# Performance work log

Hardware: AMD Instinct MI355X
Metric: run time of the kernel (lower is better)

The kernel has to match this reference:

```python
import jax, jax.numpy as jnp
import numpy as np

NEG_SLOPE = 0.2
NEG_INF = -1e9


def _gat_branch(x, src, dst, edge_type, t, W, a_src, a_dst, b):
    """Single-head PyG GATConv restricted (by masking) to edges with edge_type == t,
    with self-loops added (PyG default add_self_loops=True)."""
    N = x.shape[0]
    h = x @ W                                   # [N, out_dim]
    s = h @ a_src                               # [N] source attention term
    d = h @ a_dst                               # [N] destination attention term
    # real edges (masked by type)
    e_edge = jax.nn.leaky_relu(s[src] + d[dst], NEG_SLOPE)
    e_edge = jnp.where(edge_type == t, e_edge, NEG_INF)
    # self-loop edges i -> i
    e_self = jax.nn.leaky_relu(s + d, NEG_SLOPE)
    dst_all = jnp.concatenate([dst, jnp.arange(N)])          # [E+N]
    e_all = jnp.concatenate([e_edge, e_self])                 # [E+N]
    # softmax over incoming edges per destination node (segment softmax)
    m = jax.ops.segment_max(e_all, dst_all, num_segments=N)
    p = jnp.exp(e_all - m[dst_all])
    denom = jax.ops.segment_sum(p, dst_all, num_segments=N)
    alpha = p / denom[dst_all]                                 # [E+N]
    msg = jnp.concatenate([h[src], h], axis=0) * alpha[:, None]
    return jax.ops.segment_sum(msg, dst_all, num_segments=N) + b


def setup_inputs() -> dict:
    key = jax.random.key(0)
    ks = jax.random.split(key, 12)
    N, E, in_dim, out_dim = 100000, 1000000, 64, 64
    glorot = (6.0 / (in_dim + out_dim)) ** 0.5
    att = (6.0 / (1 + out_dim)) ** 0.5
    return {
        "x": jax.random.normal(ks[0], (N, in_dim), dtype=jnp.float32),
        "edge_index": jax.random.randint(ks[1], (2, E), 0, N),
        "edge_type": jax.random.randint(ks[2], (E,), 0, 2),
        "W_login": jax.random.uniform(ks[3], (in_dim, out_dim), jnp.float32, -glorot, glorot),
        "a_src_login": jax.random.uniform(ks[4], (out_dim,), jnp.float32, -att, att),
        "a_dst_login": jax.random.uniform(ks[5], (out_dim,), jnp.float32, -att, att),
        "b_login": jnp.zeros((out_dim,), jnp.float32),
        "W_exec": jax.random.uniform(ks[6], (in_dim, out_dim), jnp.float32, -glorot, glorot),
        "a_src_exec": jax.random.uniform(ks[7], (out_dim,), jnp.float32, -att, att),
        "a_dst_exec": jax.random.uniform(ks[8], (out_dim,), jnp.float32, -att, att),
        "b_exec": jnp.zeros((out_dim,), jnp.float32),
    }


def reference(x, edge_index, edge_type, W_login, a_src_login, a_dst_login, b_login,
              W_exec, a_src_exec, a_dst_exec, b_exec):
    src, dst = edge_index[0], edge_index[1]
    out = _gat_branch(x, src, dst, edge_type, 0, W_login, a_src_login, a_dst_login, b_login)
    out = out + _gat_branch(x, src, dst, edge_type, 1, W_exec, a_src_exec, a_dst_exec, b_exec)
    return out
```

## Files before the change

kernel.cpp:

```cpp
#include <hip/hip_runtime.h>

#define D 64
#define CAP 896
#define BINB 256

typedef unsigned short u16;
typedef __attribute__((ext_vector_type(8))) __bf16 bf16x8;
typedef __attribute__((ext_vector_type(4))) float f32x4;

__device__ __forceinline__ float lrelu(float x) { return x > 0.f ? x : 0.2f * x; }
__device__ __forceinline__ u16 f2bf(float f) {
    unsigned u = __float_as_uint(f);
    return (u16)((u + 0x7fffu + ((u >> 16) & 1u)) >> 16);
}
__device__ __forceinline__ float bf2f(u16 v) { return __uint_as_float((unsigned)v << 16); }
__device__ __forceinline__ unsigned pack2(float lo, float hi) {
    return (unsigned)f2bf(lo) | ((unsigned)f2bf(hi) << 16);
}
__device__ __forceinline__ float blo(unsigned u) { return __uint_as_float(u << 16); }
__device__ __forceinline__ float bhi(unsigned u) { return __uint_as_float(u & 0xffff0000u); }

__global__ __launch_bounds__(256) void k_gemm3(
    const float* __restrict__ x,
    const float* __restrict__ W0, const float* __restrict__ as0, const float* __restrict__ ad0,
    const float* __restrict__ W1, const float* __restrict__ as1, const float* __restrict__ ad1,
    u16* __restrict__ hb, float* __restrict__ s_tab, float* __restrict__ d_tab,
    int N, int ntiles)
{
    __shared__ u16 Wb[2][64][64];
    __shared__ u16 Xb[64][72];
    __shared__ float wsd[4][64];

    const int tid = threadIdx.x;

    for (int i = tid; i < 4096; i += 256) {
        const int k = i >> 6, n = i & 63;
        Wb[0][n][k] = f2bf(W0[i]);
        Wb[1][n][k] = f2bf(W1[i]);
    }
    {
        const int k = tid & 63;
        const int v = tid >> 6;
        const float* Ws = (v < 2) ? W0 : W1;
        const float* av = (v == 0) ? as0 : (v == 1) ? ad0 : (v == 2) ? as1 : ad1;
        float q = 0.f;
        for (int n = 0; n < 64; ++n) q = fmaf(Ws[(k << 6) + n], av[n], q);
        wsd[v][k] = q;
    }
    __syncthreads();

    const int lane = tid & 63;
    const int nl = lane & 15, quad = lane >> 4;
    const int wv = tid >> 6;

    bf16x8 bfrag[2][4][2];
#pragma unroll
    for (int br = 0; br < 2; ++br)
#pragma unroll
        for (int t = 0; t < 4; ++t)
#pragma unroll
            for (int h = 0; h < 2; ++h)
                bfrag[br][t][h] = *(const bf16x8*)&Wb[br][t * 16 + nl][h * 32 + quad * 8];

    const int rstage = tid >> 2;
    const int kc = (tid & 3) << 4;

    for (int tile = blockIdx.x; tile < ntiles; tile += gridDim.x) {
        const long n0 = (long)tile << 6;
        __syncthreads();
        {
            long row = n0 + rstage; if (row >= N) row = N - 1;
            const float4* xp = (const float4*)(x + row * D + kc);
            const float4 v0 = xp[0], v1 = xp[1], v2 = xp[2], v3 = xp[3];

            unsigned q[8];
            q[0] = pack2(v0.x, v0.y); q[1] = pack2(v0.z, v0.w);
            q[2] = pack2(v1.x, v1.y); q[3] = pack2(v1.z, v1.w);
            q[4] = pack2(v2.x, v2.y); q[5] = pack2(v2.z, v2.w);
            q[6] = pack2(v3.x, v3.y); q[7] = pack2(v3.z, v3.w);
            *(uint4*)&Xb[rstage][kc]     = make_uint4(q[0], q[1], q[2], q[3]);
            *(uint4*)&Xb[rstage][kc + 8] = make_uint4(q[4], q[5], q[6], q[7]);

            float ps[4];
#pragma unroll
            for (int v = 0; v < 4; ++v) {
                const float4* wp = (const float4*)&wsd[v][kc];
                const float4 wa = wp[0], wb = wp[1], wc = wp[2], wd = wp[3];
                float s = 0.f;
                s = fmaf(v0.x, wa.x, s); s = fmaf(v0.y, wa.y, s);
                s = fmaf(v0.z, wa.z, s); s = fmaf(v0.w, wa.w, s);
                s = fmaf(v1.x, wb.x, s); s = fmaf(v1.y, wb.y, s);
                s = fmaf(v1.z, wb.z, s); s = fmaf(v1.w, wb.w, s);
                s = fmaf(v2.x, wc.x, s); s = fmaf(v2.y, wc.y, s);
                s = fmaf(v2.z, wc.z, s); s = fmaf(v2.w, wc.w, s);
                s = fmaf(v3.x, wd.x, s); s = fmaf(v3.y, wd.y, s);
                s = fmaf(v3.z, wd.z, s); s = fmaf(v3.w, wd.w, s);
                ps[v] = s;
            }
#pragma unroll
            for (int v = 0; v < 4; ++v) {
                ps[v] += __shfl_xor(ps[v], 1, 64);
                ps[v] += __shfl_xor(ps[v], 2, 64);
            }
            const long rw = n0 + rstage;
            if ((tid & 3) == 0 && rw < N) {
                s_tab[(rw << 1)]     = ps[0]; d_tab[(rw << 1)]     = ps[1];
                s_tab[(rw << 1) | 1] = ps[2]; d_tab[(rw << 1) | 1] = ps[3];
            }
        }
        __syncthreads();

        const int rbase = wv << 4;
        const bf16x8 a0 = *(const bf16x8*)&Xb[rbase + nl][quad * 8];
        const bf16x8 a1 = *(const bf16x8*)&Xb[rbase + nl][32 + quad * 8];

        f32x4 acc[2][4];
#pragma unroll
        for (int br = 0; br < 2; ++br)
#pragma unroll
            for (int t = 0; t < 4; ++t) {
                f32x4 c = {0.f, 0.f, 0.f, 0.f};
                c = __builtin_amdgcn_mfma_f32_16x16x32_bf16(a0, bfrag[br][t][0], c, 0, 0, 0);
                c = __builtin_amdgcn_mfma_f32_16x16x32_bf16(a1, bfrag[br][t][1], c, 0, 0, 0);
                acc[br][t] = c;
            }

#pragma unroll
        for (int reg = 0; reg < 4; ++reg) {
            const long row = n0 + rbase + (quad << 2) + reg;
            if (row < N) {
#pragma unroll
                for (int br = 0; br < 2; ++br) {
                    uint2 v;
                    v.x = pack2(acc[br][0][reg], acc[br][1][reg]);
                    v.y = pack2(acc[br][2][reg], acc[br][3][reg]);
                    *(uint2*)(hb + (((row << 1) | br) << 6) + (nl << 2)) = v;
                }
            }
        }
    }
}

__global__ __launch_bounds__(256) void k_bin1(
    const int* __restrict__ src, const int* __restrict__ dst,
    const int* __restrict__ et, int* __restrict__ bktcnt,
    unsigned* __restrict__ bkt, int E, int nbk, int Eseg)
{
    extern __shared__ int cnt_l[];
    const int tid = threadIdx.x;
    for (int i = tid; i < nbk; i += 256) cnt_l[i] = 0;
    __syncthreads();

    const long e0 = (long)blockIdx.x * Eseg;
    const long e1 = min(e0 + (long)Eseg, (long)E);

    long i = e0 + tid;
    for (; i + 256 * 7 < e1; i += 256 * 8) {
        int d[8];
#pragma unroll
        for (int k = 0; k < 8; ++k) d[k] = dst[i + 256 * k];
#pragma unroll
        for (int k = 0; k < 8; ++k) atomicAdd(&cnt_l[d[k] >> 6], 1);
    }
    for (; i < e1; i += 256) atomicAdd(&cnt_l[dst[i] >> 6], 1);
    __syncthreads();

    for (int j = tid; j < nbk; j += 256) {
        const int c = cnt_l[j];
        cnt_l[j] = c ? atomicAdd(bktcnt + j, c) : 0;
    }
    __syncthreads();

    i = e0 + tid;
    for (; i + 256 * 7 < e1; i += 256 * 8) {
        int d[8];
#pragma unroll
        for (int k = 0; k < 8; ++k) d[k] = dst[i + 256 * k];
#pragma unroll
        for (int k = 0; k < 8; ++k) {
            const int bb = d[k] >> 6;
            const long ii = i + 256 * k;
            const int slot = atomicAdd(&cnt_l[bb], 1);
            if (slot < CAP)
                bkt[(long)bb * CAP + slot] =
                    ((unsigned)(d[k] & 63) << 18) | ((unsigned)src[ii] << 1) | (unsigned)et[ii];
        }
    }
    for (; i < e1; i += 256) {
        const int d = dst[i];
        const int bb = d >> 6;
        const int slot = atomicAdd(&cnt_l[bb], 1);
        if (slot < CAP)
            bkt[(long)bb * CAP + slot] =
                ((unsigned)(d & 63) << 18) | ((unsigned)src[i] << 1) | (unsigned)et[i];
    }
}

__global__ __launch_bounds__(512) void k_proc(
    const int* __restrict__ bktcnt, const unsigned* __restrict__ bkt,
    const float* __restrict__ s_tab, const float* __restrict__ d_tab,
    const u16* __restrict__ hb,
    const float* __restrict__ b0, const float* __restrict__ b1,
    float* __restrict__ out, int N)
{
    __shared__ unsigned tok[CAP];
    __shared__ int degl[64];
    __shared__ int curl[64];
    __shared__ float bsum[64];

    const int tid = threadIdx.x;
    const int b = blockIdx.x;
    const int lo = b << 6;
    const int cnt_nodes = min(64, N - lo);
    const int nb = min(bktcnt[b], CAP);

    if (tid < 64) { degl[tid] = 0; bsum[tid] = b0[tid] + b1[tid]; }
    __syncthreads();

    unsigned pr[2];
    int ns = 0;
    for (int i = tid; i < nb; i += 512) {
        const unsigned p = bkt[(long)b * CAP + i];
        pr[ns++] = p;
        atomicAdd(&degl[(p >> 18) & 63], 1);
    }
    __syncthreads();
    if (tid < 64) {
        int v = degl[tid];
        const int orig = v;
#pragma unroll
        for (int o = 1; o < 64; o <<= 1) {
            const int u = __shfl_up(v, o, 64);
            if (tid >= o) v += u;
        }
        curl[tid] = v - orig;
    }
    __syncthreads();
    for (int k = 0, i = tid; k < ns; i += 512, ++k) {
        const unsigned p = pr[k];
        const int s = atomicAdd(&curl[(p >> 18) & 63], 1);
        tok[s] = p & 0x3FFFFu;
    }
    __syncthreads();

    const int lane = tid & 63;
    const int wave = tid >> 6;
    const int q = lane >> 4;
    const int cl = lane & 15;

    for (int ni = wave; ni < cnt_nodes; ni += 8) {
        const int n = lo + ni;
        const int deg = degl[ni];
        const int off = curl[ni] - deg;
        const float d0n = d_tab[(n << 1)];
        const float d1n = d_tab[(n << 1) | 1];

        if (deg <= 62) {
            const int cnt = deg + 2;
            unsigned cmb = 0; unsigned t = 0; float e = 0.f;
            if (lane < deg) {
                cmb = tok[off + lane];
                t = cmb & 1u;
                e = lrelu(s_tab[cmb] + (t ? d1n : d0n));
            } else if (lane == deg)   { cmb = (unsigned)(n << 1);      t = 0; e = lrelu(s_tab[cmb] + d0n); }
            else if (lane == deg + 1) { cmb = (unsigned)(n << 1) | 1u; t = 1; e = lrelu(s_tab[cmb] + d1n); }

            const bool act = lane < cnt;
            const float p = act ? __expf(e) : 0.f;
            float p0 = t ? 0.f : p;
            float p1 = t ? p : 0.f;
#pragma unroll
            for (int o = 32; o; o >>= 1) {
                p0 += __shfl_xor(p0, o, 64);
                p1 += __shfl_xor(p1, o, 64);
            }
            const float a_r = act ? p / (t ? p1 : p0) : 0.f;

            float4 acc = {0.f, 0.f, 0.f, 0.f};
            const int nq = (cnt + 3) >> 2;
            int pp = 0;
            for (; pp + 1 < nq; pp += 2) {
                const int iA = (pp << 2) + q;
                const int iB = iA + 4;
                const int iBc = iB < cnt ? iB : cnt - 1;
                float aA    = __shfl(a_r, iA, 64);
                unsigned cA = __shfl(cmb, iA, 64);
                float aB    = __shfl(a_r, iBc, 64);
                unsigned cB = __shfl(cmb, iBc, 64);
                if (iB >= cnt) aB = 0.f;
                const uint2 uA = *(const uint2*)(hb + ((long)cA << 6) + (cl << 2));
                const uint2 uB = *(const uint2*)(hb + ((long)cB << 6) + (cl << 2));
                acc.x = fmaf(aA, blo(uA.x), acc.x);
                acc.y = fmaf(aA, bhi(uA.x), acc.y);
                acc.z = fmaf(aA, blo(uA.y), acc.z);
                acc.w = fmaf(aA, bhi(uA.y), acc.w);
                acc.x = fmaf(aB, blo(uB.x), acc.x);
                acc.y = fmaf(aB, bhi(uB.x), acc.y);
                acc.z = fmaf(aB, blo(uB.y), acc.z);
                acc.w = fmaf(aB, bhi(uB.y), acc.w);
            }
            if (pp < nq) {
                const int iA = (pp << 2) + q;
                const int iAc = iA < cnt ? iA : cnt - 1;
                float aA    = __shfl(a_r, iAc, 64);
                unsigned cA = __shfl(cmb, iAc, 64);
                if (iA >= cnt) aA = 0.f;
                const uint2 uA = *(const uint2*)(hb + ((long)cA << 6) + (cl << 2));
                acc.x = fmaf(aA, blo(uA.x), acc.x);
                acc.y = fmaf(aA, bhi(uA.x), acc.y);
                acc.z = fmaf(aA, blo(uA.y), acc.z);
                acc.w = fmaf(aA, bhi(uA.y), acc.w);
            }
            acc.x += __shfl_xor(acc.x, 16, 64);
            acc.y += __shfl_xor(acc.y, 16, 64);
            acc.z += __shfl_xor(acc.z, 16, 64);
            acc.w += __shfl_xor(acc.w, 16, 64);
            acc.x += __shfl_xor(acc.x, 32, 64);
            acc.y += __shfl_xor(acc.y, 32, 64);
            acc.z += __shfl_xor(acc.z, 32, 64);
            acc.w += __shfl_xor(acc.w, 32, 64);
            if (lane < 16) {
                float* op = out + ((long)n << 6);
                op[cl]      = acc.x + bsum[cl];
                op[16 + cl] = acc.y + bsum[16 + cl];
                op[32 + cl] = acc.z + bsum[32 + cl];
                op[48 + cl] = acc.w + bsum[48 + cl];
            }
        } else {
            const int oc = ((lane & 3) << 4) + (lane >> 2);
            const float es0 = lrelu(s_tab[(n << 1)] + d0n);
            const float es1 = lrelu(s_tab[(n << 1) | 1] + d1n);
            float p0 = 0.f, p1 = 0.f;
            for (int j = lane; j < deg; j += 64) {
                const unsigned c = tok[off + j];
                const float e = lrelu(s_tab[c] + ((c & 1u) ? d1n : d0n));
                if (c & 1u) p1 += __expf(e); else p0 += __expf(e);
            }
#pragma unroll
            for (int o = 32; o; o >>= 1) {
                p0 += __shfl_xor(p0, o, 64);
                p1 += __shfl_xor(p1, o, 64);
            }
            const float den0 = p0 + __expf(es0);
            const float den1 = p1 + __expf(es1);

            float acc = (__expf(es0) / den0) * bf2f(hb[((long)n << 7) + lane])
                      + (__expf(es1) / den1) * bf2f(hb[((long)n << 7) + 64 + lane]);
            for (int base = 0; base < deg; base += 64) {
                const int j = base + lane;
                unsigned ck = 0; float a = 0.f;
                if (j < deg) {
                    ck = tok[off + j];
                    const float e = lrelu(s_tab[ck] + ((ck & 1u) ? d1n : d0n));
                    a = __expf(e) / ((ck & 1u) ? den1 : den0);
                }
                const int lim = min(64, deg - base);
                for (int jj = 0; jj < lim; ++jj) {
                    const float aj = __shfl(a, jj, 64);
                    const unsigned cj = __shfl(ck, jj, 64);
                    acc = fmaf(aj, bf2f(hb[((long)cj << 6) + lane]), acc);
                }
            }
            out[((long)n << 6) + oc] = acc + bsum[oc];
        }
    }
}

extern "C" void kernel_launch(void* const* d_in, const int* in_sizes, int n_in,
                              void* d_out, int out_size, void* d_ws, size_t ws_size,
                              hipStream_t stream) {
    const float* x   = (const float*)d_in[0];
    const int*   ei  = (const int*)d_in[1];
    const int*   et  = (const int*)d_in[2];
    const float* W0  = (const float*)d_in[3];
    const float* as0 = (const float*)d_in[4];
    const float* ad0 = (const float*)d_in[5];
    const float* b0  = (const float*)d_in[6];
    const float* W1  = (const float*)d_in[7];
    const float* as1 = (const float*)d_in[8];
    const float* ad1 = (const float*)d_in[9];
    const float* b1  = (const float*)d_in[10];
    float* out = (float*)d_out;

    const int N = in_sizes[0] / D;
    const int E = in_sizes[1] / 2;
    const int* src = ei;
    const int* dst = ei + E;

    const int nbk = (N + 63) >> 6;

    char* w = (char*)d_ws;
    u16* hb = (u16*)w;            w += (size_t)2 * N * D * sizeof(u16);
    float* s_tab = (float*)w;     w += (size_t)2 * N * sizeof(float);
    float* d_tab = (float*)w;     w += (size_t)2 * N * sizeof(float);
    int* bktcnt = (int*)w;        w += (size_t)nbk * sizeof(int);
    unsigned* bkt = (unsigned*)w; w += (size_t)nbk * CAP * sizeof(unsigned);

    const int ntiles = (N + 63) / 64;
    const int Eseg = (E + BINB - 1) / BINB;

    hipMemsetAsync(bktcnt, 0, (size_t)nbk * sizeof(int), stream);
    k_gemm3<<<768, 256, 0, stream>>>(x, W0, as0, ad0, W1, as1, ad1,
                                     hb, s_tab, d_tab, N, ntiles);
    k_bin1<<<BINB, 256, (size_t)nbk * sizeof(int), stream>>>(
        src, dst, et, bktcnt, bkt, E, nbk, Eseg);
    k_proc<<<nbk, 512, 0, stream>>>(bktcnt, bkt, s_tab, d_tab, hb, b0, b1, out, N);
}
```

Baseline: 195.0 us.

## Fuse GEMM and edge binning into one front kernel; widen gather loads

Merges the projection GEMM kernel and the edge-binning kernel into a single 768-block kernel. Each block runs its GEMM tiles, then reuses the weight shared memory as local bucket counters and bins its edge segment, which removes one launch and spreads binning over more blocks. The aggregation kernel now has each lane gather 8 bf16 features with a 16-byte load instead of 4 with an 8-byte load, so 8 edges are processed per step. It also adds a nontemporal load for bucket tokens. The trade-offs are a longer shuffle reduction, more registers, and the reused shared memory (16 KB) capping nbk at 4096, which leaves little headroom above the ~1563 buckets needed here.

```diff
diff --git a/kernel.cpp b/kernel.cpp
--- a/kernel.cpp
+++ b/kernel.cpp
@@ -2,7 +2,7 @@
 
 #define D 64
 #define CAP 896
-#define BINB 256
+#define FRONT_BLKS 768
 
 typedef unsigned short u16;
 typedef __attribute__((ext_vector_type(8))) __bf16 bf16x8;
@@ -20,12 +20,14 @@
 __device__ __forceinline__ float blo(unsigned u) { return __uint_as_float(u << 16); }
 __device__ __forceinline__ float bhi(unsigned u) { return __uint_as_float(u & 0xffff0000u); }
 
-__global__ __launch_bounds__(256) void k_gemm3(
+__global__ __launch_bounds__(256) void k_front(
     const float* __restrict__ x,
     const float* __restrict__ W0, const float* __restrict__ as0, const float* __restrict__ ad0,
     const float* __restrict__ W1, const float* __restrict__ as1, const float* __restrict__ ad1,
     u16* __restrict__ hb, float* __restrict__ s_tab, float* __restrict__ d_tab,
-    int N, int ntiles)
+    const int* __restrict__ src, const int* __restrict__ dst, const int* __restrict__ et,
+    int* __restrict__ bktcnt, unsigned* __restrict__ bkt,
+    int E, int nbk, int Eseg, int N, int ntiles)
 {
     __shared__ u16 Wb[2][64][64];
     __shared__ u16 Xb[64][72];
@@ -65,7 +67,7 @@
     const int rstage = tid >> 2;
     const int kc = (tid & 3) << 4;
 
-    for (int tile = blockIdx.x; tile < ntiles; tile += gridDim.x) {
+    for (int tile = blockIdx.x; tile < ntiles; tile += FRONT_BLKS) {
         const long n0 = (long)tile << 6;
         __syncthreads();
         {
@@ -139,15 +141,9 @@
             }
         }
     }
-}
-
-__global__ __launch_bounds__(256) void k_bin1(
-    const int* __restrict__ src, const int* __restrict__ dst,
-    const int* __restrict__ et, int* __restrict__ bktcnt,
-    unsigned* __restrict__ bkt, int E, int nbk, int Eseg)
-{
-    extern __shared__ int cnt_l[];
-    const int tid = threadIdx.x;
+
+    __syncthreads();
+    int* cnt_l = (int*)&Wb[0][0][0];
     for (int i = tid; i < nbk; i += 256) cnt_l[i] = 0;
     __syncthreads();
 
@@ -220,7 +216,7 @@
     unsigned pr[2];
     int ns = 0;
     for (int i = tid; i < nb; i += 512) {
-        const unsigned p = bkt[(long)b * CAP + i];
+        const unsigned p = __builtin_nontemporal_load(&bkt[(long)b * CAP + i]);
         pr[ns++] = p;
         atomicAdd(&degl[(p >> 18) & 63], 1);
     }
@@ -245,8 +241,8 @@
 
     const int lane = tid & 63;
     const int wave = tid >> 6;
-    const int q = lane >> 4;
-    const int cl = lane & 15;
+    const int q8 = lane >> 3;
+    const int c8 = lane & 7;
 
     for (int ni = wave; ni < cnt_nodes; ni += 8) {
         const int n = lo + ni;
@@ -276,55 +272,54 @@
             }
             const float a_r = act ? p / (t ? p1 : p0) : 0.f;
 
-            float4 acc = {0.f, 0.f, 0.f, 0.f};
-            const int nq = (cnt + 3) >> 2;
+            float acc[8] = {0.f, 0.f, 0.f, 0.f, 0.f, 0.f, 0.f, 0.f};
+            const int no = (cnt + 7) >> 3;
             int pp = 0;
-            for (; pp + 1 < nq; pp += 2) {
-                const int iA = (pp << 2) + q;
-                const int iB = iA + 4;
+            for (; pp + 1 < no; pp += 2) {
+                const int iA = (pp << 3) + q8;
+                const int iB = iA + 8;
                 const int iBc = iB < cnt ? iB : cnt - 1;
                 float aA    = __shfl(a_r, iA, 64);
                 unsigned cA = __shfl(cmb, iA, 64);
                 float aB    = __shfl(a_r, iBc, 64);
                 unsigned cB = __shfl(cmb, iBc, 64);
                 if (iB >= cnt) aB = 0.f;
-                const uint2 uA = *(const uint2*)(hb + ((long)cA << 6) + (cl << 2));
-                const uint2 uB = *(const uint2*)(hb + ((long)cB << 6) + (cl << 2));
-                acc.x = fmaf(aA, blo(uA.x), acc.x);
-                acc.y = fmaf(aA, bhi(uA.x), acc.y);
-                acc.z = fmaf(aA, blo(uA.y), acc.z);
-                acc.w = fmaf(aA, bhi(uA.y), acc.w);
-                acc.x = fmaf(aB, blo(uB.x), acc.x);
-                acc.y = fmaf(aB, bhi(uB.x), acc.y);
-                acc.z = fmaf(aB, blo(uB.y), acc.z);
-                acc.w = fmaf(aB, bhi(uB.y), acc.w);
-            }
-            if (pp < nq) {
-                const int iA = (pp << 2) + q;
+                const uint4 uA = *(const uint4*)(hb + ((long)cA << 6) + (c8 << 3));
+                const uint4 uB = *(const uint4*)(hb + ((long)cB << 6) + (c8 << 3));
+                acc[0] = fmaf(aA, blo(uA.x), acc[0]); acc[1] = fmaf(aA, bhi(uA.x), acc[1]);
+                acc[2] = fmaf(aA, blo(uA.y), acc[2]); acc[3] = fmaf(aA, bhi(uA.y), acc[3]);
+                acc[4] = fmaf(aA, blo(uA.z), acc[4]); acc[5] = fmaf(aA, bhi(uA.z), acc[5]);
+                acc[6] = fmaf(aA, blo(uA.w), acc[6]); acc[7] = fmaf(aA, bhi(uA.w), acc[7]);
+                acc[0] = fmaf(aB, blo(uB.x), acc[0]); acc[1] = fmaf(aB, bhi(uB.x), acc[1]);
+                acc[2] = fmaf(aB, blo(uB.y), acc[2]); acc[3] = fmaf(aB, bhi(uB.y), acc[3]);
+                acc[4] = fmaf(aB, blo(uB.z), acc[4]); acc[5] = fmaf(aB, bhi(uB.z), acc[5]);
+                acc[6] = fmaf(aB, blo(uB.w), acc[6]); acc[7] = fmaf(aB, bhi(uB.w), acc[7]);
+            }
+            if (pp < no) {
+                const int iA = (pp << 3) + q8;
                 const int iAc = iA < cnt ? iA : cnt - 1;
                 float aA    = __shfl(a_r, iAc, 64);
                 unsigned cA = __shfl(cmb, iAc, 64);
                 if (iA >= cnt) aA = 0.f;
-                const uint2 uA = *(const uint2*)(hb + ((long)cA << 6) + (cl << 2));
-                acc.x = fmaf(aA, blo(uA.x), acc.x);
-                acc.y = fmaf(aA, bhi(uA.x), acc.y);
-                acc.z = fmaf(aA, blo(uA.y), acc.z);
-                acc.w = fmaf(aA, bhi(uA.y), acc.w);
-            }
-            acc.x += __shfl_xor(acc.x, 16, 64);
-            acc.y += __shfl_xor(acc.y, 16, 64);
-            acc.z += __shfl_xor(acc.z, 16, 64);
-            acc.w += __shfl_xor(acc.w, 16, 64);
-            acc.x += __shfl_xor(acc.x, 32, 64);
-            acc.y += __shfl_xor(acc.y, 32, 64);
-            acc.z += __shfl_xor(acc.z, 32, 64);
-            acc.w += __shfl_xor(acc.w, 32, 64);
-            if (lane < 16) {
+                const uint4 uA = *(const uint4*)(hb + ((long)cA << 6) + (c8 << 3));
+                acc[0] = fmaf(aA, blo(uA.x), acc[0]); acc[1] = fmaf(aA, bhi(uA.x), acc[1]);
+                acc[2] = fmaf(aA, blo(uA.y), acc[2]); acc[3] = fmaf(aA, bhi(uA.y), acc[3]);
+                acc[4] = fmaf(aA, blo(uA.z), acc[4]); acc[5] = fmaf(aA, bhi(uA.z), acc[5]);
+                acc[6] = fmaf(aA, blo(uA.w), acc[6]); acc[7] = fmaf(aA, bhi(uA.w), acc[7]);
+            }
+#pragma unroll
+            for (int j = 0; j < 8; ++j) {
+                acc[j] += __shfl_xor(acc[j], 8, 64);
+                acc[j] += __shfl_xor(acc[j], 16, 64);
+                acc[j] += __shfl_xor(acc[j], 32, 64);
+            }
+            if (lane < 8) {
                 float* op = out + ((long)n << 6);
-                op[cl]      = acc.x + bsum[cl];
-                op[16 + cl] = acc.y + bsum[16 + cl];
-                op[32 + cl] = acc.z + bsum[32 + cl];
-                op[48 + cl] = acc.w + bsum[48 + cl];
+                const int c2 = lane << 1;
+                *(float2*)(op + c2)      = make_float2(acc[0] + bsum[c2],      acc[4] + bsum[c2 + 1]);
+                *(float2*)(op + 16 + c2) = make_float2(acc[1] + bsum[16 + c2], acc[5] + bsum[16 + c2 + 1]);
+                *(float2*)(op + 32 + c2) = make_float2(acc[2] + bsum[32 + c2], acc[6] + bsum[32 + c2 + 1]);
+                *(float2*)(op + 48 + c2) = make_float2(acc[3] + bsum[48 + c2], acc[7] + bsum[48 + c2 + 1]);
             }
         } else {
             const int oc = ((lane & 3) << 4) + (lane >> 2);
@@ -397,12 +392,11 @@
     unsigned* bkt = (unsigned*)w; w += (size_t)nbk * CAP * sizeof(unsigned);
 
     const int ntiles = (N + 63) / 64;
-    const int Eseg = (E + BINB - 1) / BINB;
+    const int Eseg = (E + FRONT_BLKS - 1) / FRONT_BLKS;
 
     hipMemsetAsync(bktcnt, 0, (size_t)nbk * sizeof(int), stream);
-    k_gemm3<<<768, 256, 0, stream>>>(x, W0, as0, ad0, W1, as1, ad1,
-                                     hb, s_tab, d_tab, N, ntiles);
-    k_bin1<<<BINB, 256, (size_t)nbk * sizeof(int), stream>>>(
-        src, dst, et, bktcnt, bkt, E, nbk, Eseg);
+    k_front<<<FRONT_BLKS, 256, 0, stream>>>(
+        x, W0, as0, ad0, W1, as1, ad1, hb, s_tab, d_tab,
+        src, dst, et, bktcnt, bkt, E, nbk, Eseg, N, ntiles);
     k_proc<<<nbk, 512, 0, stream>>>(bktcnt, bkt, s_tab, d_tab, hb, b0, b1, out, N);
 }
```

New measurement: 207.5 us. 6.4% more time.
